# Performance work log

Measured on AMD Instinct MI355X. Metric: run time of the kernel, lower is better.

The kernel has to match this reference:

```python
import jax, jax.numpy as jnp
import numpy as np
import math

L, N, D = 1024, 64, 64
O = 1024

def setup_inputs() -> dict:
    key = jax.random.key(0)
    k1, k2 = jax.random.split(key)
    x = jax.random.normal(k1, (L, N, D), dtype=jnp.float32)
    upfold = jax.random.normal(k2, (O, N, D), dtype=jnp.float32)
    return {"x": x, "upfold": upfold}

def reference(x, upfold):
    # x: [L, N, D], upfold: [O, N, D]
    d = x.shape[-1]
    scale = 1.0 / math.sqrt(d)
    # affinities: [L, O, N]
    affinities = jnp.einsum('lnd,ond->lon', x, upfold) * scale
    # weighted sum with (sigmoid - 0.5) weights: [L, N, D]
    features = jnp.einsum('lon,ond->lnd', jax.nn.sigmoid(affinities) - 0.5, upfold)
    return features
```

## Files before the change

kernel.cpp:

```cpp
#include <hip/hip_runtime.h>
#include <stdint.h>

#define L_DIM 1024
#define N_DIM 64
#define D_DIM 64
#define O_DIM 1024
#define ND    4096
#define NT    8

typedef float    floatx16 __attribute__((ext_vector_type(16)));
typedef _Float16 half8    __attribute__((ext_vector_type(8)));
typedef _Float16 h2       __attribute__((ext_vector_type(2)));
typedef __fp16   fp16x2   __attribute__((ext_vector_type(2)));

#define BUF_STRIDE 17920

__device__ __forceinline__ uint32_t pkh2(float a, float b) {
    fp16x2 p = __builtin_amdgcn_cvt_pkrtz(a, b);
    return __builtin_bit_cast(uint32_t, p);
}

__device__ __forceinline__ half8 mk_frag(uint32_t a, uint32_t b, uint32_t c, uint32_t d) {
    union { uint32_t u[4]; half8 v; } U;
    U.u[0] = a; U.u[1] = b; U.u[2] = c; U.u[3] = d;
    return U.v;
}

__device__ __forceinline__ uint32_t psig(float s0, float s1) {
    const h2 HI = {(_Float16)41.6f,        (_Float16)41.6f};
    const h2 LO = {(_Float16)-41.6f,       (_Float16)-41.6f};
    const h2 SC = {(_Float16)0.0625f,      (_Float16)0.0625f};
    const h2 C0 = {(_Float16)0.03099238f,  (_Float16)0.03099238f};
    const h2 C1 = {(_Float16)-0.00842090f, (_Float16)-0.00842090f};
    const h2 C2 = {(_Float16)0.00151845f,  (_Float16)0.00151845f};
    const h2 C3 = {(_Float16)-1.02197e-4f, (_Float16)-1.02197e-4f};
    h2 s = __builtin_bit_cast(h2, pkh2(s0, s1));
    s = __builtin_elementwise_min(s, HI);
    s = __builtin_elementwise_max(s, LO);
    h2 ha = s * SC;
    h2 v  = ha * ha;
    h2 w  = C2 + v * C3;
    w     = C1 + v * w;
    w     = C0 + v * w;
    h2 f  = s * w;
    return __builtin_bit_cast(uint32_t, f);
}

__device__ __forceinline__ void load_tile(const float* ubase, int ot,
                                          int r8, int c, float4* va, float4* vb) {
    const float* pr = ubase + (size_t)(ot * 64 + 2 * r8) * ND + 4 * c;
    #pragma unroll
    for (int j = 0; j < 2; ++j) {
        va[j] = *(const float4*)(pr + (size_t)(32 * j) * ND);
        vb[j] = *(const float4*)(pr + (size_t)(32 * j) * ND + ND);
    }
}

__global__ void __launch_bounds__(512, 4)
corr_kernel(const float* __restrict__ x, const float* __restrict__ up,
            float* __restrict__ out)
{
    __shared__ __align__(16) unsigned char smem[4 * BUF_STRIDE];

    const int tid  = threadIdx.x;
    const int lane = tid & 63;
    const int wid  = tid >> 6;
    const int team = wid >> 2;
    const int tw   = wid & 3;
    const int l31  = lane & 31;
    const int h    = lane >> 5;
    const int ttid = tid & 255;
    const int r8   = ttid >> 4;
    const int c    = ttid & 15;
    const int n    = blockIdx.x;
    const int lb   = blockIdx.y;
    const int lw   = lb * 128 + tw * 32 + l31;

    const float* ubase = up + (size_t)n * D_DIM;
    const int ob = team * NT;
    unsigned char* tsmem = smem + team * 2 * BUF_STRIDE;

    float4 va[2], vb[2];
    load_tile(ubase, ob + 0, r8, c, va, vb);

    half8 Xf[4];
    {
        float (*Xs)[68] = (float (*)[68])smem;
        const int xr = tid >> 2;
        const int xq = tid & 3;
        const float* xsrc = x + (size_t)(lb * 128 + xr) * ND + n * D_DIM;
        #pragma unroll
        for (int j = 0; j < 4; ++j) {
            const int f4i = xq * 4 + j;
            *(float4*)&Xs[xr][4 * f4i] = *(const float4*)(xsrc + 4 * f4i);
        }
        __syncthreads();
        const int rl = tw * 32 + l31;
        #pragma unroll
        for (int kk = 0; kk < 4; ++kk) {
            float4 f1 = *(const float4*)&Xs[rl][16 * kk + 8 * h];
            float4 f2 = *(const float4*)&Xs[rl][16 * kk + 8 * h + 4];
            Xf[kk] = mk_frag(pkh2(f1.x, f1.y), pkh2(f1.z, f1.w),
                             pkh2(f2.x, f2.y), pkh2(f2.z, f2.w));
        }
        __syncthreads();
    }

    #pragma unroll
    for (int j = 0; j < 2; ++j) {
        uint16_t (*Ub)[72]  = (uint16_t (*)[72])(tsmem);
        uint32_t (*Ut2)[68] = (uint32_t (*)[68])(tsmem + 9216);
        *(uint2*)&Ub[2*r8 + 32*j][4*c] =
            make_uint2(pkh2(va[j].x, va[j].y), pkh2(va[j].z, va[j].w));
        *(uint2*)&Ub[2*r8 + 32*j + 1][4*c] =
            make_uint2(pkh2(vb[j].x, vb[j].y), pkh2(vb[j].z, vb[j].w));
        *(uint4*)&Ut2[r8 + 16*j][4*c] =
            make_uint4(pkh2(va[j].x, vb[j].x), pkh2(va[j].y, vb[j].y),
                       pkh2(va[j].z, vb[j].z), pkh2(va[j].w, vb[j].w));
    }
    load_tile(ubase, ob + 1, r8, c, va, vb);
    __syncthreads();

    floatx16 F0, F1;
    #pragma unroll
    for (int i = 0; i < 16; ++i) { F0[i] = 0.0f; F1[i] = 0.0f; }

    for (int ot = 0; ot < NT; ++ot) {
        const int b = ot & 1;
        uint16_t (*Ub)[72]   = (uint16_t (*)[72])(tsmem + b * BUF_STRIDE);
        const uint32_t* utp  = (const uint32_t*)(tsmem + b * BUF_STRIDE + 9216);
        uint16_t (*Ubn)[72]  = (uint16_t (*)[72])(tsmem + (b ^ 1) * BUF_STRIDE);
        uint32_t (*Ut2n)[68] = (uint32_t (*)[68])(tsmem + (b ^ 1) * BUF_STRIDE + 9216);

        half8 A0k[4], A1k[4];
        #pragma unroll
        for (int kk = 0; kk < 4; ++kk) {
            A0k[kk] = *(const half8*)&Ub[l31][16 * kk + 8 * h];
            A1k[kk] = *(const half8*)&Ub[32 + l31][16 * kk + 8 * h];
        }

        if (ot + 1 < NT) {
            #pragma unroll
            for (int j = 0; j < 2; ++j) {
                *(uint2*)&Ubn[2*r8 + 32*j][4*c] =
                    make_uint2(pkh2(va[j].x, va[j].y), pkh2(va[j].z, va[j].w));
                *(uint2*)&Ubn[2*r8 + 32*j + 1][4*c] =
                    make_uint2(pkh2(vb[j].x, vb[j].y), pkh2(vb[j].z, vb[j].w));
                *(uint4*)&Ut2n[r8 + 16*j][4*c] =
                    make_uint4(pkh2(va[j].x, vb[j].x), pkh2(va[j].y, vb[j].y),
                               pkh2(va[j].z, vb[j].z), pkh2(va[j].w, vb[j].w));
            }
        }
        if (ot + 2 < NT)
            load_tile(ubase, ob + ot + 2, r8, c, va, vb);

        floatx16 S0, S1;
        #pragma unroll
        for (int i = 0; i < 16; ++i) { S0[i] = 0.0f; S1[i] = 0.0f; }
        #pragma unroll
        for (int kk = 0; kk < 4; ++kk) {
            S0 = __builtin_amdgcn_mfma_f32_32x32x16_f16(A0k[kk], Xf[kk], S0, 0, 0, 0);
            S1 = __builtin_amdgcn_mfma_f32_32x32x16_f16(A1k[kk], Xf[kk], S1, 0, 0, 0);
        }

        uint32_t P[16];
        #pragma unroll
        for (int m = 0; m < 8; ++m) P[m]     = psig(S0[2*m], S0[2*m+1]);
        #pragma unroll
        for (int m = 0; m < 8; ++m) P[8 + m] = psig(S1[2*m], S1[2*m+1]);

        uint32_t R[8];
        #pragma unroll
        for (int c2 = 0; c2 < 4; ++c2) {
            const uint32_t* Q = P + (c2 >> 1) * 8;
            const int t4 = (c2 & 1) * 4;
            R[2*c2]   = __shfl_xor(h ? Q[t4]     : Q[t4 + 2], 32);
            R[2*c2+1] = __shfl_xor(h ? Q[t4 + 1] : Q[t4 + 3], 32);
        }
        #pragma unroll
        for (int c2 = 0; c2 < 4; ++c2) {
            const uint32_t* Q = P + (c2 >> 1) * 8;
            const int t4 = (c2 & 1) * 4;
            half8 B = h ? mk_frag(R[2*c2], R[2*c2+1], Q[t4 + 2], Q[t4 + 3])
                        : mk_frag(Q[t4], Q[t4 + 1], R[2*c2], R[2*c2+1]);
            const int opb = 8 * c2 + 4 * h;
            uint32_t a0[4], a1[4];
            #pragma unroll
            for (int k = 0; k < 4; ++k) {
                a0[k] = utp[(opb + k) * 68 + l31];
                a1[k] = utp[(opb + k) * 68 + 32 + l31];
            }
            half8 A0 = mk_frag(a0[0], a0[1], a0[2], a0[3]);
            half8 A1 = mk_frag(a1[0], a1[1], a1[2], a1[3]);
            F0 = __builtin_amdgcn_mfma_f32_32x32x16_f16(A0, B, F0, 0, 0, 0);
            F1 = __builtin_amdgcn_mfma_f32_32x32x16_f16(A1, B, F1, 0, 0, 0);
        }
        __syncthreads();
    }

    {
        float (*Fs)[68] = (float (*)[68])smem;
        const int row = tw * 32 + l31;
        if (team == 1) {
            #pragma unroll
            for (int q = 0; q < 4; ++q) {
                float4 a; a.x = F0[4*q]; a.y = F0[4*q+1]; a.z = F0[4*q+2]; a.w = F0[4*q+3];
                *(float4*)&Fs[row][8*q + 4*h] = a;
                float4 bq; bq.x = F1[4*q]; bq.y = F1[4*q+1]; bq.z = F1[4*q+2]; bq.w = F1[4*q+3];
                *(float4*)&Fs[row][32 + 8*q + 4*h] = bq;
            }
        }
        __syncthreads();
        if (team == 0) {
            float* op = out + (size_t)lw * ND + n * D_DIM;
            #pragma unroll
            for (int q = 0; q < 4; ++q) {
                float4 t0 = *(const float4*)&Fs[row][8*q + 4*h];
                float4 a; a.x = F0[4*q]   + t0.x; a.y = F0[4*q+1] + t0.y;
                          a.z = F0[4*q+2] + t0.z; a.w = F0[4*q+3] + t0.w;
                *(float4*)(op + 8*q + 4*h) = a;
                float4 t1 = *(const float4*)&Fs[row][32 + 8*q + 4*h];
                float4 bq; bq.x = F1[4*q]   + t1.x; bq.y = F1[4*q+1] + t1.y;
                           bq.z = F1[4*q+2] + t1.z; bq.w = F1[4*q+3] + t1.w;
                *(float4*)(op + 32 + 8*q + 4*h) = bq;
            }
        }
    }
}

extern "C" void kernel_launch(void* const* d_in, const int* in_sizes, int n_in,
                              void* d_out, int out_size, void* d_ws, size_t ws_size,
                              hipStream_t stream)
{
    const float* x  = (const float*)d_in[0];
    const float* up = (const float*)d_in[1];
    float* out      = (float*)d_out;
    dim3 grid(N_DIM, L_DIM / 128);
    corr_kernel<<<grid, dim3(512), 0, stream>>>(x, up, out);
}
```

Baseline: 101.9 us.

## Precompute fp16 upfold tile images and stream them into LDS via global_load_lds

Adds a pre-pass kernel that converts each upfold tile to fp16 once, in both its normal and transposed LDS layout, and writes it to workspace. The main kernel then copies these ready-made images straight into LDS with asynchronous global_load_lds, double-buffered per team. This removes the per-block fp32 loads, conversions and scattered LDS stores that were repeated across all 8 L-blocks. The cost is an extra launch and a workspace round trip. A fallback path keeps the old kernel when no workspace is provided.

```diff
diff --git a/kernel.cpp b/kernel.cpp
--- a/kernel.cpp
+++ b/kernel.cpp
@@ -13,7 +13,14 @@
 typedef _Float16 h2       __attribute__((ext_vector_type(2)));
 typedef __fp16   fp16x2   __attribute__((ext_vector_type(2)));
 
-#define BUF_STRIDE 17920
+#define IMG_TILE 19
+#undef IMG_TILE
+#define UB_BYTES  9216
+#define UTT_BYTES 9728
+#define IMG_BYTES (UB_BYTES + UTT_BYTES)
+#define WS_NEEDED ((size_t)N_DIM * 16 * IMG_BYTES)
+
+#define BUF_STRIDE_FB 17920
 
 __device__ __forceinline__ uint32_t pkh2(float a, float b) {
     fp16x2 p = __builtin_amdgcn_cvt_pkrtz(a, b);
@@ -56,11 +63,204 @@
     }
 }
 
+__device__ __forceinline__ void gll16(const unsigned char* g, unsigned char* l) {
+    __builtin_amdgcn_global_load_lds(
+        (const __attribute__((address_space(1))) void*)g,
+        (__attribute__((address_space(3))) void*)l, 16, 0, 0);
+}
+
+__global__ void __launch_bounds__(256)
+conv_kernel(const float* __restrict__ up, unsigned char* __restrict__ img)
+{
+    const int tid = threadIdx.x;
+    const int r8  = tid >> 4;
+    const int c   = tid & 15;
+    const int n   = blockIdx.x;
+    const int ot  = blockIdx.y;
+
+    const float* ubase = up + (size_t)n * D_DIM;
+    float4 va[2], vb[2];
+    load_tile(ubase, ot, r8, c, va, vb);
+
+    unsigned char* tb = img + (size_t)(n * 16 + ot) * IMG_BYTES;
+    uint16_t (*Ub)[72]  = (uint16_t (*)[72])tb;
+    uint32_t (*UtT)[38] = (uint32_t (*)[38])(tb + UB_BYTES);
+
+    #pragma unroll
+    for (int j = 0; j < 2; ++j) {
+        *(uint2*)&Ub[2*r8 + 32*j][4*c] =
+            make_uint2(pkh2(va[j].x, va[j].y), pkh2(va[j].z, va[j].w));
+        *(uint2*)&Ub[2*r8 + 32*j + 1][4*c] =
+            make_uint2(pkh2(vb[j].x, vb[j].y), pkh2(vb[j].z, vb[j].w));
+        const int op = r8 + 16*j;
+        UtT[4*c + 0][op] = pkh2(va[j].x, vb[j].x);
+        UtT[4*c + 1][op] = pkh2(va[j].y, vb[j].y);
+        UtT[4*c + 2][op] = pkh2(va[j].z, vb[j].z);
+        UtT[4*c + 3][op] = pkh2(va[j].w, vb[j].w);
+    }
+}
+
 __global__ void __launch_bounds__(512, 4)
-corr_kernel(const float* __restrict__ x, const float* __restrict__ up,
-            float* __restrict__ out)
+corr_kernel_g(const float* __restrict__ x, const unsigned char* __restrict__ img,
+              float* __restrict__ out)
 {
-    __shared__ __align__(16) unsigned char smem[4 * BUF_STRIDE];
+    __shared__ __align__(16) unsigned char smem[4 * IMG_BYTES];
+
+    const int tid  = threadIdx.x;
+    const int lane = tid & 63;
+    const int wid  = tid >> 6;
+    const int team = wid >> 2;
+    const int tw   = wid & 3;
+    const int l31  = lane & 31;
+    const int h    = lane >> 5;
+    const int ttid = tid & 255;
+    const int n    = blockIdx.x;
+    const int lb   = blockIdx.y;
+    const int lw   = lb * 128 + tw * 32 + l31;
+
+    const int ob = team * NT;
+    unsigned char* tsmem = smem + team * 2 * IMG_BYTES;
+    const unsigned char* gimg = img + (size_t)n * 16 * IMG_BYTES;
+
+    half8 Xf[4];
+    {
+        float (*Xs)[68] = (float (*)[68])smem;
+        const int xr = tid >> 2;
+        const int xq = tid & 3;
+        const float* xsrc = x + (size_t)(lb * 128 + xr) * ND + n * D_DIM;
+        #pragma unroll
+        for (int j = 0; j < 4; ++j) {
+            const int f4i = xq * 4 + j;
+            *(float4*)&Xs[xr][4 * f4i] = *(const float4*)(xsrc + 4 * f4i);
+        }
+        __syncthreads();
+        const int rl = tw * 32 + l31;
+        #pragma unroll
+        for (int kk = 0; kk < 4; ++kk) {
+            float4 f1 = *(const float4*)&Xs[rl][16 * kk + 8 * h];
+            float4 f2 = *(const float4*)&Xs[rl][16 * kk + 8 * h + 4];
+            Xf[kk] = mk_frag(pkh2(f1.x, f1.y), pkh2(f1.z, f1.w),
+                             pkh2(f2.x, f2.y), pkh2(f2.z, f2.w));
+        }
+        __syncthreads();
+    }
+
+    {
+        const unsigned char* g0 = gimg + (size_t)ob * IMG_BYTES;
+        #pragma unroll
+        for (int i = 0; i < 4; ++i)
+            gll16(g0 + ttid * 16 + i * 4096, tsmem + tw * 1024 + i * 4096);
+        if (ttid < 160)
+            gll16(g0 + ttid * 16 + 16384, tsmem + tw * 1024 + 16384);
+    }
+    __syncthreads();
+
+    floatx16 F0, F1;
+    #pragma unroll
+    for (int i = 0; i < 16; ++i) { F0[i] = 0.0f; F1[i] = 0.0f; }
+
+    for (int ot = 0; ot < NT; ++ot) {
+        const int b = ot & 1;
+        const unsigned char* bufc = tsmem + b * IMG_BYTES;
+        unsigned char*       bufn = tsmem + (b ^ 1) * IMG_BYTES;
+        const uint16_t (*Ub)[72] = (const uint16_t (*)[72])bufc;
+        const uint32_t* utT      = (const uint32_t*)(bufc + UB_BYTES);
+
+        if (ot + 1 < NT) {
+            const unsigned char* gn = gimg + (size_t)(ob + ot + 1) * IMG_BYTES;
+            #pragma unroll
+            for (int i = 0; i < 4; ++i)
+                gll16(gn + ttid * 16 + i * 4096, bufn + tw * 1024 + i * 4096);
+            if (ttid < 160)
+                gll16(gn + ttid * 16 + 16384, bufn + tw * 1024 + 16384);
+        }
+
+        half8 A0k[4], A1k[4];
+        #pragma unroll
+        for (int kk = 0; kk < 4; ++kk) {
+            A0k[kk] = *(const half8*)&Ub[l31][16 * kk + 8 * h];
+            A1k[kk] = *(const half8*)&Ub[32 + l31][16 * kk + 8 * h];
+        }
+
+        floatx16 S0, S1;
+        #pragma unroll
+        for (int i = 0; i < 16; ++i) { S0[i] = 0.0f; S1[i] = 0.0f; }
+        #pragma unroll
+        for (int kk = 0; kk < 4; ++kk) {
+            S0 = __builtin_amdgcn_mfma_f32_32x32x16_f16(A0k[kk], Xf[kk], S0, 0, 0, 0);
+            S1 = __builtin_amdgcn_mfma_f32_32x32x16_f16(A1k[kk], Xf[kk], S1, 0, 0, 0);
+        }
+
+        uint32_t P[16];
+        #pragma unroll
+        for (int m = 0; m < 8; ++m) P[m]     = psig(S0[2*m], S0[2*m+1]);
+        #pragma unroll
+        for (int m = 0; m < 8; ++m) P[8 + m] = psig(S1[2*m], S1[2*m+1]);
+
+        uint32_t R[8];
+        #pragma unroll
+        for (int c2 = 0; c2 < 4; ++c2) {
+            const uint32_t* Q = P + (c2 >> 1) * 8;
+            const int t4 = (c2 & 1) * 4;
+            R[2*c2]   = __shfl_xor(h ? Q[t4]     : Q[t4 + 2], 32);
+            R[2*c2+1] = __shfl_xor(h ? Q[t4 + 1] : Q[t4 + 3], 32);
+        }
+        #pragma unroll
+        for (int c2 = 0; c2 < 4; ++c2) {
+            const uint32_t* Q = P + (c2 >> 1) * 8;
+            const int t4 = (c2 & 1) * 4;
+            half8 B = h ? mk_frag(R[2*c2], R[2*c2+1], Q[t4 + 2], Q[t4 + 3])
+                        : mk_frag(Q[t4], Q[t4 + 1], R[2*c2], R[2*c2+1]);
+            const int opb = 8 * c2 + 4 * h;
+            const uint32_t* r0 = utT + l31 * 38;
+            const uint32_t* r1 = utT + (32 + l31) * 38;
+            uint2 q0 = *(const uint2*)(r0 + opb);
+            uint2 q1 = *(const uint2*)(r0 + opb + 2);
+            uint2 q2 = *(const uint2*)(r1 + opb);
+            uint2 q3 = *(const uint2*)(r1 + opb + 2);
+            half8 A0 = mk_frag(q0.x, q0.y, q1.x, q1.y);
+            half8 A1 = mk_frag(q2.x, q2.y, q3.x, q3.y);
+            F0 = __builtin_amdgcn_mfma_f32_32x32x16_f16(A0, B, F0, 0, 0, 0);
+            F1 = __builtin_amdgcn_mfma_f32_32x32x16_f16(A1, B, F1, 0, 0, 0);
+        }
+        __syncthreads();
+    }
+
+    {
+        float (*Fs)[68] = (float (*)[68])smem;
+        const int row = tw * 32 + l31;
+        if (team == 1) {
+            #pragma unroll
+            for (int q = 0; q < 4; ++q) {
+                float4 a; a.x = F0[4*q]; a.y = F0[4*q+1]; a.z = F0[4*q+2]; a.w = F0[4*q+3];
+                *(float4*)&Fs[row][8*q + 4*h] = a;
+                float4 bq; bq.x = F1[4*q]; bq.y = F1[4*q+1]; bq.z = F1[4*q+2]; bq.w = F1[4*q+3];
+                *(float4*)&Fs[row][32 + 8*q + 4*h] = bq;
+            }
+        }
+        __syncthreads();
+        if (team == 0) {
+            float* op = out + (size_t)lw * ND + n * D_DIM;
+            #pragma unroll
+            for (int q = 0; q < 4; ++q) {
+                float4 t0 = *(const float4*)&Fs[row][8*q + 4*h];
+                float4 a; a.x = F0[4*q]   + t0.x; a.y = F0[4*q+1] + t0.y;
+                          a.z = F0[4*q+2] + t0.z; a.w = F0[4*q+3] + t0.w;
+                *(float4*)(op + 8*q + 4*h) = a;
+                float4 t1 = *(const float4*)&Fs[row][32 + 8*q + 4*h];
+                float4 bq; bq.x = F1[4*q]   + t1.x; bq.y = F1[4*q+1] + t1.y;
+                           bq.z = F1[4*q+2] + t1.z; bq.w = F1[4*q+3] + t1.w;
+                *(float4*)(op + 32 + 8*q + 4*h) = bq;
+            }
+        }
+    }
+}
+
+__global__ void __launch_bounds__(512, 4)
+corr_kernel_fb(const float* __restrict__ x, const float* __restrict__ up,
+               float* __restrict__ out)
+{
+    __shared__ __align__(16) unsigned char smem[4 * BUF_STRIDE_FB];
 
     const int tid  = threadIdx.x;
     const int lane = tid & 63;
@@ -78,7 +278,7 @@
 
     const float* ubase = up + (size_t)n * D_DIM;
     const int ob = team * NT;
-    unsigned char* tsmem = smem + team * 2 * BUF_STRIDE;
+    unsigned char* tsmem = smem + team * 2 * BUF_STRIDE_FB;
 
     float4 va[2], vb[2];
     load_tile(ubase, ob + 0, r8, c, va, vb);
@@ -127,10 +327,10 @@
 
     for (int ot = 0; ot < NT; ++ot) {
         const int b = ot & 1;
-        uint16_t (*Ub)[72]   = (uint16_t (*)[72])(tsmem + b * BUF_STRIDE);
-        const uint32_t* utp  = (const uint32_t*)(tsmem + b * BUF_STRIDE + 9216);
-        uint16_t (*Ubn)[72]  = (uint16_t (*)[72])(tsmem + (b ^ 1) * BUF_STRIDE);
-        uint32_t (*Ut2n)[68] = (uint32_t (*)[68])(tsmem + (b ^ 1) * BUF_STRIDE + 9216);
+        uint16_t (*Ub)[72]   = (uint16_t (*)[72])(tsmem + b * BUF_STRIDE_FB);
+        const uint32_t* utp  = (const uint32_t*)(tsmem + b * BUF_STRIDE_FB + 9216);
+        uint16_t (*Ubn)[72]  = (uint16_t (*)[72])(tsmem + (b ^ 1) * BUF_STRIDE_FB);
+        uint32_t (*Ut2n)[68] = (uint32_t (*)[68])(tsmem + (b ^ 1) * BUF_STRIDE_FB + 9216);
 
         half8 A0k[4], A1k[4];
         #pragma unroll
@@ -235,6 +435,12 @@
     const float* x  = (const float*)d_in[0];
     const float* up = (const float*)d_in[1];
     float* out      = (float*)d_out;
-    dim3 grid(N_DIM, L_DIM / 128);
-    corr_kernel<<<grid, dim3(512), 0, stream>>>(x, up, out);
-}
+
+    if (d_ws != nullptr && ws_size >= WS_NEEDED) {
+        unsigned char* img = (unsigned char*)d_ws;
+        conv_kernel<<<dim3(N_DIM, 16), dim3(256), 0, stream>>>(up, img);
+        corr_kernel_g<<<dim3(N_DIM, L_DIM / 128), dim3(512), 0, stream>>>(x, img, out);
+    } else {
+        corr_kernel_fb<<<dim3(N_DIM, L_DIM / 128), dim3(512), 0, stream>>>(x, up, out);
+    }
+}
```

Result: slower. 109.5 us (+7.4%).
